# Performance work log

Hardware: AMD Instinct MI355X
Metric: run time of the kernel (lower is better)

The kernel has to match this reference:

```python
import jax, jax.numpy as jnp
import numpy as np

N_NODES = 50000
N_EDGES = 800000
D_IN = 64
D_OUT = 64


def setup_inputs() -> dict:
    key = jax.random.key(0)
    k1, k2, k3, k4 = jax.random.split(key, 4)
    x = jax.random.normal(k1, (N_NODES, D_IN), dtype=jnp.float32)
    edge_index = jax.random.randint(k2, (2, N_EDGES), 0, N_NODES, dtype=jnp.int64)
    scale = np.sqrt(1.0 / D_IN).astype(np.float32)
    W_msg = jax.random.normal(k3, (D_OUT, D_IN), dtype=jnp.float32) * scale
    W_self = jax.random.normal(k4, (D_OUT, D_IN), dtype=jnp.float32) * scale
    b_msg = jnp.zeros((D_OUT,), dtype=jnp.float32)
    b_self = jnp.zeros((D_OUT,), dtype=jnp.float32)
    return {"x": x, "edge_index": edge_index, "W_msg": W_msg, "b_msg": b_msg,
            "W_self": W_self, "b_self": b_self}


def reference(x, edge_index, W_msg, b_msg, W_self, b_self):
    row, col = edge_index[0], edge_index[1]
    n = x.shape[0]
    # message projection on all source nodes, then gather per edge
    msgs_src = x @ W_msg.T + b_msg            # [N, D_OUT]
    per_edge = msgs_src[row]                  # [E, D_OUT] gather
    # scatter-mean into destination nodes
    summed = jax.ops.segment_sum(per_edge, col, num_segments=n)          # [N, D_OUT]
    counts = jax.ops.segment_sum(jnp.ones_like(col, dtype=x.dtype), col,
                                 num_segments=n)                         # [N]
    agg = summed / jnp.maximum(counts, 1.0)[:, None]
    self_out = x @ W_self.T + b_self
    return self_out + agg
```

## Files before the change

### kernel.cpp

```cpp
#include <hip/hip_runtime.h>

constexpr int N_NODES = 50000;
constexpr int N_EDGES = 800000;
constexpr int D = 64;
constexpr int NB = (N_NODES + 63) / 64;
constexpr int BUCKET_CAP = 1280;

typedef __attribute__((ext_vector_type(8))) short short8;
typedef __attribute__((ext_vector_type(4))) float f32x4;

static __device__ inline unsigned short f2bf(float f) {
    unsigned u = __float_as_uint(f);
    unsigned r = (u + 0x7FFFu + ((u >> 16) & 1u)) >> 16;
    return (unsigned short)r;
}
static __device__ inline unsigned pack2(float lo, float hi) {
    return (unsigned)f2bf(lo) | ((unsigned)f2bf(hi) << 16);
}
static __device__ inline float bf2f(unsigned short b) {
    return __uint_as_float((unsigned)b << 16);
}

constexpr unsigned DUMMY_ENT = 64u << 16;
constexpr float FIX_SCALE    = 65536.0f;
constexpr float FIX_INV      = 1.0f / 65536.0f;

__global__ __launch_bounds__(256) void k_prep(
    const float* __restrict__ x, unsigned short* __restrict__ xb,
    const float* __restrict__ W_msg, const float* __restrict__ W_self,
    unsigned short* __restrict__ B_packed, unsigned* __restrict__ cursor)
{
    int tid = threadIdx.x;
    int gid = blockIdx.x * 256 + tid;

    for (int t = gid; t < N_NODES * D / 4; t += 512 * 256) {
        float4 v = ((const float4*)x)[t];
        uint2 p;
        p.x = pack2(v.x, v.y);
        p.y = pack2(v.z, v.w);
        ((uint2*)xb)[t] = p;
    }
    if (blockIdx.x == 0) {
        for (int idx = tid; idx < 64 * 128; idx += 256) {
            int n = idx >> 7;
            int k = idx & 127;
            float v = (k < 64) ? W_self[n * 64 + k] : W_msg[n * 64 + (k - 64)];
            B_packed[idx] = f2bf(v);
        }
    } else if (blockIdx.x == 1) {
        for (int b = tid; b < NB; b += 256)
            cursor[b] = (unsigned)b * BUCKET_CAP;
    }
}

constexpr int BIN_BLOCKS = 128;
constexpr int EDGES_PER_BIN_BLOCK = (N_EDGES + BIN_BLOCKS - 1) / BIN_BLOCKS;

__global__ __launch_bounds__(512) void k_bin_place(
    const int* __restrict__ edge_index,
    unsigned* __restrict__ g_cursor, unsigned* __restrict__ bucket_data)
{
    __shared__ unsigned lcount[NB];
    __shared__ unsigned lbase[NB];

    int tid = threadIdx.x;
    int e0 = blockIdx.x * EDGES_PER_BIN_BLOCK;
    int e1 = min(e0 + EDGES_PER_BIN_BLOCK, N_EDGES);

    for (int b = tid; b < NB; b += 512) lcount[b] = 0u;
    __syncthreads();

    for (int e = e0 + tid; e < e1; e += 512)
        atomicAdd(&lcount[edge_index[N_EDGES + e] >> 6], 1u);
    __syncthreads();

    for (int b = tid; b < NB; b += 512) {
        unsigned c = lcount[b];
        lbase[b] = c ? atomicAdd(&g_cursor[b], c) : 0u;
    }
    __syncthreads();
    for (int b = tid; b < NB; b += 512) lcount[b] = 0u;
    __syncthreads();

    for (int e = e0 + tid; e < e1; e += 512) {
        int dst = edge_index[N_EDGES + e];
        int src = edge_index[e];
        int b = dst >> 6;
        unsigned off = atomicAdd(&lcount[b], 1u);
        bucket_data[lbase[b] + off] = (unsigned)src | ((unsigned)(dst & 63) << 16);
    }
}

constexpr int A_STRIDE = 136;

__global__ __launch_bounds__(512) void k_fused(
    const unsigned short* __restrict__ x_bf16,
    const unsigned short* __restrict__ B_packed,
    const float* __restrict__ b_msg, const float* __restrict__ b_self,
    const unsigned* __restrict__ cursor,
    const unsigned* __restrict__ bucket_data,
    float* __restrict__ out)
{
    __shared__ __align__(16) unsigned short A_sh[64 * A_STRIDE];
    __shared__ __align__(16) unsigned short ubuf[64 * A_STRIDE];
    __shared__ unsigned deg[64];

    unsigned* acci = (unsigned*)ubuf;

    int tid = threadIdx.x;
    int r0 = blockIdx.x * 64;

    for (int i = tid; i < 65 * 64; i += 512) acci[i] = 0u;
    if (tid < 64) deg[tid] = 0u;
    for (int idx = tid; idx < 64 * 16; idx += 512) {
        int row = idx >> 4;
        int c   = idx & 15;
        int g   = r0 + row;
        uint2 v = make_uint2(0u, 0u);
        if (g < N_NODES) v = *(const uint2*)&x_bf16[g * D + c * 4];
        *(uint2*)&A_sh[row * A_STRIDE + c * 4] = v;
    }
    __syncthreads();

    int w    = tid >> 6;
    int lane = tid & 63;
    unsigned start = (unsigned)blockIdx.x * BUCKET_CAP;
    unsigned end   = cursor[blockIdx.x];

    int my_deg = 0;

    for (unsigned base = start + 64u * (unsigned)w; base < end; base += 512u) {
        unsigned idxe = base + (unsigned)lane;
        unsigned entv = (idxe < end) ? bucket_data[idxe] : DUMMY_ENT;
        int enti = (int)entv;
        #pragma unroll
        for (int j0 = 0; j0 < 64; j0 += 8) {
            float    v[8];
            unsigned dd[8];
            #pragma unroll
            for (int jj = 0; jj < 8; ++jj) {
                unsigned e = (unsigned)__builtin_amdgcn_readlane(enti, j0 + jj);
                dd[jj] = e >> 16;
                v[jj]  = bf2f(x_bf16[((e & 0xFFFFu) << 6) + (unsigned)lane]);
            }
            #pragma unroll
            for (int jj = 0; jj < 8; ++jj) {
                int vi = (int)(v[jj] * FIX_SCALE);
                atomicAdd(&acci[(dd[jj] << 6) + (unsigned)lane], (unsigned)vi);
                my_deg += ((unsigned)lane == dd[jj]) ? 1 : 0;
            }
        }
    }
    atomicAdd(&deg[lane], (unsigned)my_deg);
    __syncthreads();

    for (int idx = tid; idx < 64 * 16; idx += 512) {
        int row = idx >> 4;
        int c   = idx & 15;
        unsigned dg = deg[row];
        float inv = dg ? (FIX_INV / (float)dg) : 0.0f;
        const int* ap = (const int*)&acci[row * 64 + c * 4];
        uint2 p;
        p.x = pack2((float)ap[0] * inv, (float)ap[1] * inv);
        p.y = pack2((float)ap[2] * inv, (float)ap[3] * inv);
        *(uint2*)&A_sh[row * A_STRIDE + 64 + c * 4] = p;
    }
    __syncthreads();

    for (int idx = tid; idx < 64 * 32; idx += 512) {
        int n = idx >> 5;
        int c = idx & 31;
        uint2 v = *(const uint2*)&B_packed[n * 128 + c * 4];
        *(uint2*)&ubuf[n * A_STRIDE + c * 4] = v;
    }
    __syncthreads();

    int wm   = w & 3;
    int ng   = (w >> 2) * 2;
    int quad = lane >> 4;
    int l15  = lane & 15;

    f32x4 accr[2] = {{0.f,0.f,0.f,0.f},{0.f,0.f,0.f,0.f}};

    #pragma unroll
    for (int k0 = 0; k0 < 128; k0 += 32) {
        short8 a = *(const short8*)&A_sh[(16 * wm + l15) * A_STRIDE + k0 + quad * 8];
        #pragma unroll
        for (int t = 0; t < 2; ++t) {
            short8 b = *(const short8*)&ubuf[(16 * (ng + t) + l15) * A_STRIDE + k0 + quad * 8];
            accr[t] = __builtin_amdgcn_mfma_f32_16x16x32_bf16(a, b, accr[t], 0, 0, 0);
        }
    }

    #pragma unroll
    for (int t = 0; t < 2; ++t) {
        int col = (ng + t) * 16 + l15;
        float bs = b_self[col];
        float bm = b_msg[col];
        #pragma unroll
        for (int r = 0; r < 4; ++r) {
            int lrow = 16 * wm + quad * 4 + r;
            int grow = r0 + lrow;
            if (grow < N_NODES) {
                float vv = accr[t][r] + bs + (deg[lrow] > 0u ? bm : 0.0f);
                out[grow * D + col] = vv;
            }
        }
    }
}

extern "C" void kernel_launch(void* const* d_in, const int* in_sizes, int n_in,
                              void* d_out, int out_size, void* d_ws, size_t ws_size,
                              hipStream_t stream) {
    const float* x      = (const float*)d_in[0];
    const int*   edges  = (const int*)  d_in[1];
    const float* W_msg  = (const float*)d_in[2];
    const float* b_msg  = (const float*)d_in[3];
    const float* W_self = (const float*)d_in[4];
    const float* b_self = (const float*)d_in[5];
    float*       out    = (float*)d_out;

    char* ws = (char*)d_ws;
    unsigned*       cursor      = (unsigned*)(ws + 0);
    unsigned short* B_packed    = (unsigned short*)(ws + 4096);
    unsigned*       bucket_data = (unsigned*)(ws + 20480);
    unsigned short* x_bf16      = (unsigned short*)(ws + 4030464);

    k_prep<<<512, 256, 0, stream>>>(x, x_bf16, W_msg, W_self, B_packed, cursor);
    k_bin_place<<<BIN_BLOCKS, 512, 0, stream>>>(edges, cursor, bucket_data);
    k_fused<<<NB, 512, 0, stream>>>(x_bf16, B_packed, b_msg, b_self,
                                    cursor, bucket_data, out);
}
```

Baseline: 125.3 us.

## Sort bucket edges by destination in LDS and aggregate per-row in registers

Replaces the per-edge LDS fixed-point atomic accumulation with a per-block counting sort of edges by destination row (count, prefix scan, scatter into shared memory). Each wave then handles eight destination rows, gathering source rows as vectorized ushort4 loads, summing in float registers and reducing across quarter-waves with shuffles. This removes 64 LDS atomics per edge and the fixed-point conversion, at the cost of extra passes over bucket data, two more barriers, and possible load imbalance across rows of differing degree.

```diff
diff --git a/kernel.cpp b/kernel.cpp
--- a/kernel.cpp
+++ b/kernel.cpp
@@ -20,10 +20,6 @@
 static __device__ inline float bf2f(unsigned short b) {
     return __uint_as_float((unsigned)b << 16);
 }
-
-constexpr unsigned DUMMY_ENT = 64u << 16;
-constexpr float FIX_SCALE    = 65536.0f;
-constexpr float FIX_INV      = 1.0f / 65536.0f;
 
 __global__ __launch_bounds__(256) void k_prep(
     const float* __restrict__ x, unsigned short* __restrict__ xb,
@@ -102,16 +98,21 @@
     float* __restrict__ out)
 {
     __shared__ __align__(16) unsigned short A_sh[64 * A_STRIDE];
-    __shared__ __align__(16) unsigned short ubuf[64 * A_STRIDE];
-    __shared__ unsigned deg[64];
-
-    unsigned* acci = (unsigned*)ubuf;
-
-    int tid = threadIdx.x;
-    int r0 = blockIdx.x * 64;
-
-    for (int i = tid; i < 65 * 64; i += 512) acci[i] = 0u;
-    if (tid < 64) deg[tid] = 0u;
+    __shared__ __align__(16) unsigned short B_sh[64 * A_STRIDE];
+    __shared__ unsigned short sorted_sh[BUCKET_CAP];
+    __shared__ unsigned cnt_sh[64];
+    __shared__ unsigned off_sh[64];
+    __shared__ unsigned woff_sh[64];
+
+    int tid  = threadIdx.x;
+    int w    = tid >> 6;
+    int lane = tid & 63;
+    int r0   = blockIdx.x * 64;
+
+    unsigned start = (unsigned)blockIdx.x * BUCKET_CAP;
+    unsigned end   = cursor[blockIdx.x];
+
+    if (tid < 64) cnt_sh[tid] = 0u;
     for (int idx = tid; idx < 64 * 16; idx += 512) {
         int row = idx >> 4;
         int c   = idx & 15;
@@ -120,58 +121,76 @@
         if (g < N_NODES) v = *(const uint2*)&x_bf16[g * D + c * 4];
         *(uint2*)&A_sh[row * A_STRIDE + c * 4] = v;
     }
-    __syncthreads();
-
-    int w    = tid >> 6;
-    int lane = tid & 63;
-    unsigned start = (unsigned)blockIdx.x * BUCKET_CAP;
-    unsigned end   = cursor[blockIdx.x];
-
-    int my_deg = 0;
-
-    for (unsigned base = start + 64u * (unsigned)w; base < end; base += 512u) {
-        unsigned idxe = base + (unsigned)lane;
-        unsigned entv = (idxe < end) ? bucket_data[idxe] : DUMMY_ENT;
-        int enti = (int)entv;
-        #pragma unroll
-        for (int j0 = 0; j0 < 64; j0 += 8) {
-            float    v[8];
-            unsigned dd[8];
-            #pragma unroll
-            for (int jj = 0; jj < 8; ++jj) {
-                unsigned e = (unsigned)__builtin_amdgcn_readlane(enti, j0 + jj);
-                dd[jj] = e >> 16;
-                v[jj]  = bf2f(x_bf16[((e & 0xFFFFu) << 6) + (unsigned)lane]);
-            }
-            #pragma unroll
-            for (int jj = 0; jj < 8; ++jj) {
-                int vi = (int)(v[jj] * FIX_SCALE);
-                atomicAdd(&acci[(dd[jj] << 6) + (unsigned)lane], (unsigned)vi);
-                my_deg += ((unsigned)lane == dd[jj]) ? 1 : 0;
-            }
-        }
-    }
-    atomicAdd(&deg[lane], (unsigned)my_deg);
-    __syncthreads();
-
-    for (int idx = tid; idx < 64 * 16; idx += 512) {
-        int row = idx >> 4;
-        int c   = idx & 15;
-        unsigned dg = deg[row];
-        float inv = dg ? (FIX_INV / (float)dg) : 0.0f;
-        const int* ap = (const int*)&acci[row * 64 + c * 4];
-        uint2 p;
-        p.x = pack2((float)ap[0] * inv, (float)ap[1] * inv);
-        p.y = pack2((float)ap[2] * inv, (float)ap[3] * inv);
-        *(uint2*)&A_sh[row * A_STRIDE + 64 + c * 4] = p;
-    }
-    __syncthreads();
-
     for (int idx = tid; idx < 64 * 32; idx += 512) {
         int n = idx >> 5;
         int c = idx & 31;
         uint2 v = *(const uint2*)&B_packed[n * 128 + c * 4];
-        *(uint2*)&ubuf[n * A_STRIDE + c * 4] = v;
+        *(uint2*)&B_sh[n * A_STRIDE + c * 4] = v;
+    }
+    __syncthreads();
+
+    for (unsigned i = start + tid; i < end; i += 512u)
+        atomicAdd(&cnt_sh[bucket_data[i] >> 16], 1u);
+    __syncthreads();
+
+    if (tid < 64) {
+        unsigned c = cnt_sh[tid];
+        unsigned xsum = c;
+        #pragma unroll
+        for (int s = 1; s < 64; s <<= 1) {
+            unsigned v = (unsigned)__shfl_up((int)xsum, s);
+            if (lane >= s) xsum += v;
+        }
+        off_sh[tid]  = xsum - c;
+        woff_sh[tid] = xsum - c;
+    }
+    __syncthreads();
+
+    for (unsigned i = start + tid; i < end; i += 512u) {
+        unsigned e = bucket_data[i];
+        unsigned slot = atomicAdd(&woff_sh[e >> 16], 1u);
+        sorted_sh[slot] = (unsigned short)(e & 0xFFFFu);
+    }
+    __syncthreads();
+
+    int Q = lane >> 4;
+    int f = lane & 15;
+
+    for (int i = 0; i < 8; ++i) {
+        int lrow = w * 8 + i;
+        unsigned s0 = off_sh[lrow];
+        unsigned dc = cnt_sh[lrow];
+        unsigned e_end = s0 + dc;
+
+        float a0 = 0.f, a1 = 0.f, a2 = 0.f, a3 = 0.f;
+        for (unsigned b = s0; b < e_end; b += 8u) {
+            unsigned i0 = b + (unsigned)Q;
+            unsigned i1 = b + 4u + (unsigned)Q;
+            unsigned src0 = (i0 < e_end) ? (unsigned)sorted_sh[i0] : 0u;
+            unsigned src1 = (i1 < e_end) ? (unsigned)sorted_sh[i1] : 0u;
+            ushort4 rv0 = *(const ushort4*)&x_bf16[(src0 << 6) + 4u * (unsigned)f];
+            ushort4 rv1 = *(const ushort4*)&x_bf16[(src1 << 6) + 4u * (unsigned)f];
+            if (i0 < e_end) {
+                a0 += bf2f(rv0.x); a1 += bf2f(rv0.y);
+                a2 += bf2f(rv0.z); a3 += bf2f(rv0.w);
+            }
+            if (i1 < e_end) {
+                a0 += bf2f(rv1.x); a1 += bf2f(rv1.y);
+                a2 += bf2f(rv1.z); a3 += bf2f(rv1.w);
+            }
+        }
+        a0 += __shfl_xor(a0, 16); a1 += __shfl_xor(a1, 16);
+        a2 += __shfl_xor(a2, 16); a3 += __shfl_xor(a3, 16);
+        a0 += __shfl_xor(a0, 32); a1 += __shfl_xor(a1, 32);
+        a2 += __shfl_xor(a2, 32); a3 += __shfl_xor(a3, 32);
+
+        if (Q == 0) {
+            float inv = dc ? 1.0f / (float)dc : 0.0f;
+            uint2 p;
+            p.x = pack2(a0 * inv, a1 * inv);
+            p.y = pack2(a2 * inv, a3 * inv);
+            *(uint2*)&A_sh[lrow * A_STRIDE + 64 + 4 * f] = p;
+        }
     }
     __syncthreads();
 
@@ -187,7 +206,7 @@
         short8 a = *(const short8*)&A_sh[(16 * wm + l15) * A_STRIDE + k0 + quad * 8];
         #pragma unroll
         for (int t = 0; t < 2; ++t) {
-            short8 b = *(const short8*)&ubuf[(16 * (ng + t) + l15) * A_STRIDE + k0 + quad * 8];
+            short8 b = *(const short8*)&B_sh[(16 * (ng + t) + l15) * A_STRIDE + k0 + quad * 8];
             accr[t] = __builtin_amdgcn_mfma_f32_16x16x32_bf16(a, b, accr[t], 0, 0, 0);
         }
     }
@@ -202,7 +221,7 @@
             int lrow = 16 * wm + quad * 4 + r;
             int grow = r0 + lrow;
             if (grow < N_NODES) {
-                float vv = accr[t][r] + bs + (deg[lrow] > 0u ? bm : 0.0f);
+                float vv = accr[t][r] + bs + (cnt_sh[lrow] > 0u ? bm : 0.0f);
                 out[grow * D + col] = vv;
             }
         }
```

After: 123.4 us. About the same (-1.5%).
